# Optimization experiments

Hardware: AMD Instinct MI355X
Metric: run time of the kernel (lower is better)

## Reference

```python
import jax, jax.numpy as jnp
import numpy as np

B, IN, OUT = 4096, 2048, 2048
GRID_SIZE, SPLINE_ORDER, Q_LEVELS = 5, 3, 64
N_COEFF = GRID_SIZE + SPLINE_ORDER  # 8


def setup_inputs() -> dict:
    key = jax.random.key(0)
    k1, k2, k3 = jax.random.split(key, 3)
    x = jax.random.uniform(k1, (B, IN), dtype=jnp.float32, minval=-1.0, maxval=1.0)
    # kaiming_uniform_(a=sqrt(5)) -> bound = 1/sqrt(in_features)
    bound = 1.0 / np.sqrt(IN)
    base_weight = jax.random.uniform(k2, (OUT, IN), dtype=jnp.float32, minval=-bound, maxval=bound)
    spline_weight = 0.1 * jax.random.normal(k3, (OUT, IN, N_COEFF), dtype=jnp.float32)
    h = 2.0 / GRID_SIZE
    grid_1d = jnp.arange(-SPLINE_ORDER, GRID_SIZE + SPLINE_ORDER + 1, dtype=jnp.float32) * h - 1.0
    grid = jnp.broadcast_to(grid_1d, (IN, grid_1d.shape[0]))  # [in, grid+2k+1]=[in,12]
    return {"x": x, "base_weight": base_weight, "spline_weight": spline_weight, "grid": grid}


def b_splines(x, grid, k):
    # x: [b, in], grid: [in, n_knots] -> bases: [b, in, n_knots-1-k]
    xe = x[:, :, None]           # [b, in, 1]
    g = grid[None, :, :]         # [1, in, n_knots]
    bases = ((xe >= g[:, :, :-1]) & (xe < g[:, :, 1:])).astype(x.dtype)
    for p in range(1, k + 1):
        t_i = g[:, :, : -1 - p]
        t_i_p = g[:, :, p:-1]
        term1 = (xe - t_i) / (t_i_p - t_i + 1e-8) * bases[:, :, :-1]
        t_i_1 = g[:, :, 1:-p]
        t_i_p_1 = g[:, :, p + 1:]
        term2 = (t_i_p_1 - xe) / (t_i_p_1 - t_i_1 + 1e-8) * bases[:, :, 1:]
        bases = term1 + term2
    return bases


def quantize_ste(w, levels):
    scale = levels / 2.0
    q = jnp.round(w * scale) / scale
    # straight-through estimator: identity gradient
    return w + jax.lax.stop_gradient(q - w)


def reference(x, base_weight, spline_weight, grid) -> jnp.ndarray:
    base_output = x @ base_weight.T                       # [b, out]
    basis = b_splines(x, grid, SPLINE_ORDER)              # [b, in, 8]
    q_weight = quantize_ste(spline_weight, Q_LEVELS)      # [out, in, 8]
    spline_output = jnp.einsum('bic,oic->bo', basis, q_weight)
    return base_output + spline_output
```

## Files before the change

kernel.cpp:

```cpp
#include <hip/hip_runtime.h>
#include <stdint.h>

#define B_DIM   4096
#define IN_DIM  2048
#define OUT_DIM 2048
#define NC      8
#define KTOT    (IN_DIM * NC)
#define KHALF   (KTOT / 2)

typedef __bf16 bf16x8 __attribute__((ext_vector_type(8)));
typedef float  floatx4 __attribute__((ext_vector_type(4)));
typedef unsigned short ushortx8 __attribute__((ext_vector_type(8)));

__device__ __forceinline__ unsigned short f2bf(float f) {
  unsigned int u = __float_as_uint(f);
  return (unsigned short)((u + 0x7FFFu + ((u >> 16) & 1u)) >> 16);
}

__device__ __forceinline__ void load_lds16(const void* g, void* l) {
  __builtin_amdgcn_global_load_lds(
      (const __attribute__((address_space(1))) void*)g,
      (__attribute__((address_space(3))) void*)l, 16, 0, 0);
}

__global__ __launch_bounds__(256) void build_A(const float* __restrict__ x,
                                               const float* __restrict__ grid,
                                               unsigned short* __restrict__ Abuf) {
  __shared__ float g[12];
  __shared__ float rec[3][12];
  int t = threadIdx.x;
  if (t < 12) g[t] = grid[t];
  __syncthreads();
  if (t < 36) {
    int p = t / 12 + 1, j = t % 12;
    if (j + p <= 11) rec[p - 1][j] = 1.0f / (g[j + p] - g[j] + 1e-8f);
  }
  __syncthreads();
  int idx = blockIdx.x * 256 + t;
  float xv = x[idx];
  float bs[11];
#pragma unroll
  for (int j = 0; j < 11; ++j)
    bs[j] = (xv >= g[j] && xv < g[j + 1]) ? 1.0f : 0.0f;
#pragma unroll
  for (int p = 1; p <= 3; ++p) {
#pragma unroll
    for (int j = 0; j + p < 11; ++j) {
      float t1 = (xv - g[j])         * rec[p - 1][j];
      float t2 = (g[j + p + 1] - xv) * rec[p - 1][j + 1];
      bs[j] = t1 * bs[j] + t2 * bs[j + 1];
    }
  }
  ushortx8 pk;
#pragma unroll
  for (int c = 0; c < 8; ++c) pk[c] = f2bf(bs[c]);
  *(ushortx8*)&Abuf[(size_t)idx * 8] = pk;
}

__global__ __launch_bounds__(256) void build_B(const float* __restrict__ sw,
                                               const float* __restrict__ bw,
                                               unsigned short* __restrict__ Bbuf) {
  int idx = blockIdx.x * 256 + threadIdx.x;
  const float4* swv = (const float4*)sw;
  float4 w0 = swv[(size_t)idx * 2];
  float4 w1 = swv[(size_t)idx * 2 + 1];
  float bwv = bw[idx];
  ushortx8 pk;
  pk[0] = f2bf(fmaf(-1.4f, bwv, rintf(w0.x * 32.f) * 0.03125f));
  pk[1] = f2bf(fmaf(-1.0f, bwv, rintf(w0.y * 32.f) * 0.03125f));
  pk[2] = f2bf(fmaf(-0.6f, bwv, rintf(w0.z * 32.f) * 0.03125f));
  pk[3] = f2bf(fmaf(-0.2f, bwv, rintf(w0.w * 32.f) * 0.03125f));
  pk[4] = f2bf(fmaf( 0.2f, bwv, rintf(w1.x * 32.f) * 0.03125f));
  pk[5] = f2bf(fmaf( 0.6f, bwv, rintf(w1.y * 32.f) * 0.03125f));
  pk[6] = f2bf(fmaf( 1.0f, bwv, rintf(w1.z * 32.f) * 0.03125f));
  pk[7] = f2bf(fmaf( 1.4f, bwv, rintf(w1.w * 32.f) * 0.03125f));
  *(ushortx8*)&Bbuf[(size_t)idx * 8] = pk;
}

__global__ __launch_bounds__(512, 2) void gemm256(const unsigned short* __restrict__ A,
                                                  const unsigned short* __restrict__ Bm,
                                                  float* __restrict__ C,
                                                  int klen) {
  __shared__ unsigned short lds[65536];

  const int tid  = threadIdx.x;
  const int wid  = tid >> 6;
  const int lane = tid & 63;
  const int wr = wid >> 2, wc = wid & 3;
  const int lm = lane & 15, lq = lane >> 4;

  const int s01 = (lq ^ (lm & 3)) * 8;
  const int sk0 = ((lm >> 2) & 1) * 32;
  const int sk1 = 32 - sk0;

  int lid = blockIdx.y * gridDim.x + blockIdx.x;
  lid = (lid & 7) * 16 + (lid >> 3);
  const int col0  = (lid & 7) * 256;
  const int row0  = (lid >> 3) * 256;
  const int kbase = blockIdx.z * klen;

  const int srow = lane >> 3;
  const int scg  = ((lane & 7) ^ srow) * 8;

  size_t offA[2][2], offB[2][2];
  int    dstA[2][2], dstB[2][2];
#pragma unroll
  for (int m = 0; m < 2; ++m)
#pragma unroll
    for (int q = 0; q < 2; ++q) {
      int rs = q * 128 + m * 64 + wid * 8;
      offA[m][q] = (size_t)(row0 + rs + srow) * KTOT + scg;
      dstA[m][q] = rs * 64;
    }
#pragma unroll
  for (int n = 0; n < 2; ++n)
#pragma unroll
    for (int q = 0; q < 2; ++q) {
      int g  = q * 8 + wid;
      int rs = ((g >> 2) * 2 + n) * 32 + (g & 3) * 8;
      offB[n][q] = (size_t)(col0 + rs + srow) * KTOT + scg;
      dstB[n][q] = rs * 64;
    }

#define STAGE_A(m, d, kp) do {                                                   \
    load_lds16(A + offA[m][0] + (kp), &lds[(d) * 32768 + dstA[m][0]]);           \
    load_lds16(A + offA[m][1] + (kp), &lds[(d) * 32768 + dstA[m][1]]);           \
  } while (0)
#define STAGE_B(n, d, kp) do {                                                   \
    load_lds16(Bm + offB[n][0] + (kp), &lds[(d) * 32768 + 16384 + dstB[n][0]]);  \
    load_lds16(Bm + offB[n][1] + (kp), &lds[(d) * 32768 + 16384 + dstB[n][1]]);  \
  } while (0)

#define VM4 asm volatile("s_waitcnt vmcnt(4)" ::: "memory")
#define VM2 asm volatile("s_waitcnt vmcnt(2)" ::: "memory")
#define VM0 asm volatile("s_waitcnt vmcnt(0)" ::: "memory")
#define NOWAIT ((void)0)

  const unsigned short* ldsA0 = lds + (wr * 128 + lm) * 64 + s01;
  const unsigned short* ldsB0 = lds + 16384 + (wc * 64 + lm) * 64 + s01;

  floatx4 acc[8][4];
#pragma unroll
  for (int i = 0; i < 8; ++i)
#pragma unroll
    for (int j = 0; j < 4; ++j) acc[i][j] = floatx4{0.f, 0.f, 0.f, 0.f};

  STAGE_A(0, 0, kbase);
  STAGE_B(0, 0, kbase);
  STAGE_B(1, 0, kbase);
  STAGE_A(1, 0, kbase);
  asm volatile("s_waitcnt vmcnt(4)" ::: "memory");
  __builtin_amdgcn_s_barrier();
  __builtin_amdgcn_sched_barrier(0);

#define RD_A(pA, mh) do {                                                        \
    _Pragma("unroll") for (int m_ = 0; m_ < 4; ++m_) {                           \
      af_[m_][0] = *(const bf16x8*)((pA) + (mh) * 4096 + m_ * 1024 + sk0);       \
      af_[m_][1] = *(const bf16x8*)((pA) + (mh) * 4096 + m_ * 1024 + sk1);       \
    }                                                                            \
  } while (0)
#define RD_B(pB, dst, nh) do {                                                   \
    _Pragma("unroll") for (int n_ = 0; n_ < 2; ++n_) {                           \
      dst[n_][0] = *(const bf16x8*)((pB) + (nh) * 2048 + n_ * 1024 + sk0);       \
      dst[n_][1] = *(const bf16x8*)((pB) + (nh) * 2048 + n_ * 1024 + sk1);       \
    }                                                                            \
  } while (0)
#define MM(mh, nh, bfr)                                                          \
    _Pragma("unroll") for (int m_ = 0; m_ < 4; ++m_)                             \
      _Pragma("unroll") for (int n_ = 0; n_ < 2; ++n_)                           \
        _Pragma("unroll") for (int k_ = 0; k_ < 2; ++k_)                         \
          acc[(mh) * 4 + m_][(nh) * 2 + n_] =                                    \
              __builtin_amdgcn_mfma_f32_16x16x32_bf16(                           \
                  af_[m_][k_], bfr[n_][k_],                                      \
                  acc[(mh) * 4 + m_][(nh) * 2 + n_], 0, 0, 0)
#define BAR1 do { __builtin_amdgcn_s_barrier();                                  \
    asm volatile("s_waitcnt lgkmcnt(0)" ::: "memory");                           \
    __builtin_amdgcn_sched_barrier(0);                                           \
    __builtin_amdgcn_s_setprio(1); } while (0)
#define BAR2(W) do { __builtin_amdgcn_s_setprio(0); W;                           \
    __builtin_amdgcn_s_barrier();                                                \
    __builtin_amdgcn_sched_barrier(0); } while (0)

  const int NT = klen / 64;
  int kp = kbase + 64;
  for (int t = 0; t < NT - 1; ++t) {
    const int dB_ = t & 1, dN_ = dB_ ^ 1;
    const unsigned short* pA = ldsA0 + dB_ * 32768;
    const unsigned short* pB = ldsB0 + dB_ * 32768;
    bf16x8 af_[4][2], bf0_[2][2], bf1_[2][2];
    RD_A(pA, 0); RD_B(pB, bf0_, 0); STAGE_A(0, dN_, kp);
    BAR1; MM(0, 0, bf0_); BAR2(VM4);
    RD_B(pB, bf1_, 1); STAGE_B(0, dN_, kp);
    BAR1; MM(0, 1, bf1_); BAR2(VM4);
    RD_A(pA, 1); STAGE_B(1, dN_, kp);
    BAR1; MM(1, 1, bf1_); BAR2(NOWAIT);
    STAGE_A(1, dN_, kp);
    BAR1; MM(1, 0, bf0_); BAR2(VM4);
    kp += 64;
  }
  {
    const int dB_ = (NT - 1) & 1;
    const unsigned short* pA = ldsA0 + dB_ * 32768;
    const unsigned short* pB = ldsB0 + dB_ * 32768;
    bf16x8 af_[4][2], bf0_[2][2], bf1_[2][2];
    RD_A(pA, 0); RD_B(pB, bf0_, 0);
    BAR1; MM(0, 0, bf0_); BAR2(VM2);
    RD_B(pB, bf1_, 1);
    BAR1; MM(0, 1, bf1_); BAR2(VM0);
    RD_A(pA, 1);
    BAR1; MM(1, 1, bf1_); BAR2(NOWAIT);
    BAR1; MM(1, 0, bf0_); BAR2(NOWAIT);
  }
#undef RD_A
#undef RD_B
#undef MM
#undef BAR1
#undef BAR2
#undef STAGE_A
#undef STAGE_B
#undef VM4
#undef VM2
#undef VM0
#undef NOWAIT

#pragma unroll
  for (int mf = 0; mf < 8; ++mf) {
    int rr = row0 + wr * 128 + mf * 16 + lq * 4;
#pragma unroll
    for (int nf = 0; nf < 4; ++nf) {
      int cc = col0 + wc * 64 + nf * 16 + lm;
#pragma unroll
      for (int q = 0; q < 4; ++q)
        atomicAdd(&C[(size_t)(rr + q) * OUT_DIM + cc], acc[mf][nf][q]);
    }
  }
}

extern "C" void kernel_launch(void* const* d_in, const int* in_sizes, int n_in,
                              void* d_out, int out_size, void* d_ws, size_t ws_size,
                              hipStream_t stream) {
  const float* x    = (const float*)d_in[0];
  const float* bw   = (const float*)d_in[1];
  const float* sw   = (const float*)d_in[2];
  const float* grid = (const float*)d_in[3];
  float* out = (float*)d_out;

  unsigned short* Abuf = (unsigned short*)d_ws;
  unsigned short* Bbuf = Abuf + (size_t)B_DIM * KTOT;

  hipLaunchKernelGGL(build_A, dim3(B_DIM * IN_DIM / 256), dim3(256), 0, stream,
                     x, grid, Abuf);
  hipLaunchKernelGGL(build_B, dim3(OUT_DIM * IN_DIM / 256), dim3(256), 0, stream,
                     sw, bw, Bbuf);
  hipLaunchKernelGGL(gemm256, dim3(OUT_DIM / 256, B_DIM / 256, 2), dim3(512),
                     0, stream, Abuf, Bbuf, out, KHALF);
}
```

Before: 522.6 us.

## Replace split-K atomics with partial buffers plus reduce, restructure barrier scheduling

The split-K GEMM now has each K-half write plain stores to its own output buffer (the real output or a workspace partial), and a separate vectorized reduce kernel adds the two. This replaces the float atomics, and any zeroing of the output they needed. The main loop also changes barrier placement: the two barriers per phase become one, the vmcnt wait moves before it, and the priority boost now wraps only the MFMA block. This adds an extra 32 MB read/write pass for the reduce, and falls back to a non-split launch when the workspace is too small.

```diff
diff --git a/kernel.cpp b/kernel.cpp
--- a/kernel.cpp
+++ b/kernel.cpp
@@ -79,7 +79,8 @@
 
 __global__ __launch_bounds__(512, 2) void gemm256(const unsigned short* __restrict__ A,
                                                   const unsigned short* __restrict__ Bm,
-                                                  float* __restrict__ C,
+                                                  float* __restrict__ C0,
+                                                  float* __restrict__ C1,
                                                   int klen) {
   __shared__ unsigned short lds[65536];
 
@@ -173,13 +174,11 @@
               __builtin_amdgcn_mfma_f32_16x16x32_bf16(                           \
                   af_[m_][k_], bfr[n_][k_],                                      \
                   acc[(mh) * 4 + m_][(nh) * 2 + n_], 0, 0, 0)
-#define BAR1 do { __builtin_amdgcn_s_barrier();                                  \
+#define BARX do { __builtin_amdgcn_s_barrier();                                  \
     asm volatile("s_waitcnt lgkmcnt(0)" ::: "memory");                           \
-    __builtin_amdgcn_sched_barrier(0);                                           \
-    __builtin_amdgcn_s_setprio(1); } while (0)
-#define BAR2(W) do { __builtin_amdgcn_s_setprio(0); W;                           \
-    __builtin_amdgcn_s_barrier();                                                \
     __builtin_amdgcn_sched_barrier(0); } while (0)
+#define MMP(mh, nh, bfr) do { __builtin_amdgcn_s_setprio(1);                     \
+    MM(mh, nh, bfr); __builtin_amdgcn_s_setprio(0); } while (0)
 
   const int NT = klen / 64;
   int kp = kbase + 64;
@@ -188,14 +187,14 @@
     const unsigned short* pA = ldsA0 + dB_ * 32768;
     const unsigned short* pB = ldsB0 + dB_ * 32768;
     bf16x8 af_[4][2], bf0_[2][2], bf1_[2][2];
-    RD_A(pA, 0); RD_B(pB, bf0_, 0); STAGE_A(0, dN_, kp);
-    BAR1; MM(0, 0, bf0_); BAR2(VM4);
-    RD_B(pB, bf1_, 1); STAGE_B(0, dN_, kp);
-    BAR1; MM(0, 1, bf1_); BAR2(VM4);
-    RD_A(pA, 1); STAGE_B(1, dN_, kp);
-    BAR1; MM(1, 1, bf1_); BAR2(NOWAIT);
-    STAGE_A(1, dN_, kp);
-    BAR1; MM(1, 0, bf0_); BAR2(VM4);
+    RD_A(pA, 0); RD_B(pB, bf0_, 0); STAGE_A(0, dN_, kp); VM4; BARX;
+    MMP(0, 0, bf0_);
+    RD_B(pB, bf1_, 1); STAGE_B(0, dN_, kp); VM4; BARX;
+    MMP(0, 1, bf1_);
+    RD_A(pA, 1); STAGE_B(1, dN_, kp); BARX;
+    MMP(1, 1, bf1_);
+    STAGE_A(1, dN_, kp); VM4; BARX;
+    MMP(1, 0, bf0_);
     kp += 64;
   }
   {
@@ -203,19 +202,19 @@
     const unsigned short* pA = ldsA0 + dB_ * 32768;
     const unsigned short* pB = ldsB0 + dB_ * 32768;
     bf16x8 af_[4][2], bf0_[2][2], bf1_[2][2];
-    RD_A(pA, 0); RD_B(pB, bf0_, 0);
-    BAR1; MM(0, 0, bf0_); BAR2(VM2);
-    RD_B(pB, bf1_, 1);
-    BAR1; MM(0, 1, bf1_); BAR2(VM0);
-    RD_A(pA, 1);
-    BAR1; MM(1, 1, bf1_); BAR2(NOWAIT);
-    BAR1; MM(1, 0, bf0_); BAR2(NOWAIT);
+    RD_A(pA, 0); RD_B(pB, bf0_, 0); VM2; BARX;
+    MMP(0, 0, bf0_);
+    RD_B(pB, bf1_, 1); VM0; BARX;
+    MMP(0, 1, bf1_);
+    RD_A(pA, 1); BARX;
+    MMP(1, 1, bf1_);
+    MMP(1, 0, bf0_);
   }
 #undef RD_A
 #undef RD_B
 #undef MM
-#undef BAR1
-#undef BAR2
+#undef MMP
+#undef BARX
 #undef STAGE_A
 #undef STAGE_B
 #undef VM4
@@ -223,6 +222,7 @@
 #undef VM0
 #undef NOWAIT
 
+  float* __restrict__ C = blockIdx.z ? C1 : C0;
 #pragma unroll
   for (int mf = 0; mf < 8; ++mf) {
     int rr = row0 + wr * 128 + mf * 16 + lq * 4;
@@ -231,9 +231,18 @@
       int cc = col0 + wc * 64 + nf * 16 + lm;
 #pragma unroll
       for (int q = 0; q < 4; ++q)
-        atomicAdd(&C[(size_t)(rr + q) * OUT_DIM + cc], acc[mf][nf][q]);
-    }
-  }
+        C[(size_t)(rr + q) * OUT_DIM + cc] = acc[mf][nf][q];
+    }
+  }
+}
+
+__global__ __launch_bounds__(256) void reduce_add(float* __restrict__ out,
+                                                  const float* __restrict__ part) {
+  int i = blockIdx.x * 256 + threadIdx.x;
+  float4 a = ((const float4*)out)[i];
+  float4 p = ((const float4*)part)[i];
+  a.x += p.x; a.y += p.y; a.z += p.z; a.w += p.w;
+  ((float4*)out)[i] = a;
 }
 
 extern "C" void kernel_launch(void* const* d_in, const int* in_sizes, int n_in,
@@ -247,11 +256,22 @@
 
   unsigned short* Abuf = (unsigned short*)d_ws;
   unsigned short* Bbuf = Abuf + (size_t)B_DIM * KTOT;
+  float* Cpart = (float*)(Bbuf + (size_t)OUT_DIM * KTOT);
+  const size_t need_split =
+      ((size_t)B_DIM + OUT_DIM) * KTOT * 2 + (size_t)B_DIM * OUT_DIM * 4;
+  const bool split = ws_size >= need_split;
 
   hipLaunchKernelGGL(build_A, dim3(B_DIM * IN_DIM / 256), dim3(256), 0, stream,
                      x, grid, Abuf);
   hipLaunchKernelGGL(build_B, dim3(OUT_DIM * IN_DIM / 256), dim3(256), 0, stream,
                      sw, bw, Bbuf);
-  hipLaunchKernelGGL(gemm256, dim3(OUT_DIM / 256, B_DIM / 256, 2), dim3(512),
-                     0, stream, Abuf, Bbuf, out, KHALF);
-}
+  if (split) {
+    hipLaunchKernelGGL(gemm256, dim3(OUT_DIM / 256, B_DIM / 256, 2), dim3(512),
+                       0, stream, Abuf, Bbuf, out, Cpart, KHALF);
+    hipLaunchKernelGGL(reduce_add, dim3(B_DIM * OUT_DIM / 4 / 256), dim3(256),
+                       0, stream, out, Cpart);
+  } else {
+    hipLaunchKernelGGL(gemm256, dim3(OUT_DIM / 256, B_DIM / 256, 1), dim3(512),
+                       0, stream, Abuf, Bbuf, out, (float*)nullptr, KTOT);
+  }
+}
```

Measured after the change: 513.7 us. No clear change (-1.7%).
